# Kernel optimization log

Hardware: AMD Instinct MI355X
Metric: run time of the kernel (lower is better)

Reference implementation:

```python
import jax, jax.numpy as jnp
import numpy as np

B, T, D = 16, 2048, 256
WINDOW = 128


def setup_inputs() -> dict:
    key = jax.random.key(0)
    ks = jax.random.split(key, 6)
    scale = 1.0 / np.sqrt(D)
    return {
        "x": jax.random.normal(ks[0], (B, T, D), dtype=jnp.float32),
        "Wq": jax.random.normal(ks[1], (D, D), dtype=jnp.float32) * scale,
        "Wk": jax.random.normal(ks[2], (D, D), dtype=jnp.float32) * scale,
        "Wv": jax.random.normal(ks[3], (D, D), dtype=jnp.float32) * scale,
        "Wo": jax.random.normal(ks[4], (D, D), dtype=jnp.float32) * scale,
        "w_bias": jax.random.normal(ks[5], (T, T), dtype=jnp.float32) * 0.1,
        "window": WINDOW,
    }


def reference(x, Wq, Wk, Wv, Wo, w_bias, window):
    # x: [B,T,D]; w_bias: [T,T] learned pairwise position bias.
    T_ = x.shape[1]
    q = jnp.einsum("btd,de->bte", x, Wq)
    k = jnp.einsum("btd,de->bte", x, Wk)
    v = jnp.einsum("btd,de->bte", x, Wv)

    # AFT-Local: bias is zeroed outside the local band |t - t'| < window,
    # but ALL positions still contribute (with bias 0) to the weighted sum.
    idx = jnp.arange(T_)
    band = jnp.abs(idx[:, None] - idx[None, :]) < window  # [T,T] bool
    w_local = jnp.where(band, w_bias, 0.0)

    # Stable exponentials: the num/den ratio is invariant to per-row shifts
    # of w and per-(b,d) shifts of k.
    w_stable = w_local - jnp.max(w_local, axis=1, keepdims=True)
    k_stable = k - jnp.max(k, axis=1, keepdims=True)
    expw = jnp.exp(w_stable)  # [T,T]
    expk = jnp.exp(k_stable)  # [B,T,D]

    num = jnp.einsum("ts,bsd->btd", expw, expk * v)
    den = jnp.einsum("ts,bsd->btd", expw, expk)
    y = jax.nn.sigmoid(q) * (num / den)
    return jnp.einsum("btd,de->bte", y, Wo)
```

## Files before the change

### kernel.cpp

```cpp
#include <hip/hip_runtime.h>
#include <math.h>

#define B_ 16
#define T_ 2048
#define D_ 256
#define W_ 128
#define M_ (B_*T_)

typedef __attribute__((ext_vector_type(8))) short bf16x8;
typedef __attribute__((ext_vector_type(4))) float f32x4;
typedef unsigned short u16;

static __device__ __forceinline__ u16 f32_bf16_rne(float f) {
    unsigned int u = __float_as_uint(f);
    u += 0x7FFF + ((u >> 16) & 1);
    return (u16)(u >> 16);
}
static __device__ __forceinline__ float bf16_f32(u16 h) {
    return __uint_as_float(((unsigned int)h) << 16);
}

__global__ __launch_bounds__(256) void aft_split_wT(
    const float* __restrict__ Wq, const float* __restrict__ Wk,
    const float* __restrict__ Wv, const float* __restrict__ Wo,
    u16* __restrict__ Wth, u16* __restrict__ Wkl)
{
    const float* Ws[4] = {Wq, Wk, Wv, Wo};
    const float* W = Ws[blockIdx.x];
    const int n  = blockIdx.y * 16 + (threadIdx.x >> 4);
    const int k0 = (threadIdx.x & 15) * 16;
    size_t obase = ((size_t)blockIdx.x * 256 + n) * 256 + k0;
    #pragma unroll 4
    for (int j = 0; j < 16; ++j) {
        float v = W[(size_t)(k0 + j) * 256 + n];
        u16 h = f32_bf16_rne(v);
        Wth[obase + j] = h;
        if (blockIdx.x == 1)
            Wkl[(size_t)n * 256 + k0 + j] = f32_bf16_rne(v - bf16_f32(h));
    }
}

__global__ void aft_ewb(const float* __restrict__ wb, u16* __restrict__ EWb)
{
    const int t = blockIdx.x;
    const int j = threadIdx.x;
    const int s = (t & ~63) - 128 + j;
    const int dlt = s - t;
    float v = 0.f;
    if (s >= 0 && s < T_ && dlt > -W_ && dlt < W_)
        v = expf(wb[(size_t)t * T_ + s]) - 1.0f;
    EWb[(size_t)t * 320 + j] = f32_bf16_rne(v);
}

__global__ __launch_bounds__(256) void aft_qkv_mfma(
    const float* __restrict__ x,
    const u16* __restrict__ Wth, const u16* __restrict__ Wkl,
    u16* __restrict__ ekT, u16* __restrict__ sigqT)
{
    __shared__ alignas(16) u16 sm[20480];
    u16* Ah = sm;
    u16* Al = sm + 5120;
    u16* Bs = sm + 10240;
    u16* Tr = sm;

    const int tid  = threadIdx.x;
    const int row0 = blockIdx.x * 128;
    const int col0 = blockIdx.y * 64;
    const int b    = row0 >> 11;
    const int t0g  = row0 & (T_ - 1);
    const int lane = tid & 63;
    const int wid  = tid >> 6;
    const int wm   = (wid & 1) * 64;
    const int wn   = (wid >> 1) * 32;
    const int qd   = lane >> 4;
    const int r    = lane & 15;

    f32x4 accq[4][2], acck[4][2], accv[4][2];
    #pragma unroll
    for (int i = 0; i < 4; ++i)
        #pragma unroll
        for (int j = 0; j < 2; ++j) {
            accq[i][j] = (f32x4){0.f, 0.f, 0.f, 0.f};
            acck[i][j] = accq[i][j];
            accv[i][j] = accq[i][j];
        }

    const int am   = tid >> 1;
    const int akh  = (tid & 1) * 16;
    const int brow = tid >> 2;
    const int bseg = (tid & 3) * 8;

    for (int k0 = 0; k0 < D_; k0 += 32) {
        {
            size_t g = (size_t)(row0 + am) * D_ + k0 + akh;
            union { ushort4 s4[4]; u16 h[16]; } H, L;
            #pragma unroll
            for (int c = 0; c < 4; ++c) {
                float4 v = *(const float4*)&x[g + c * 4];
                float vv[4] = {v.x, v.y, v.z, v.w};
                #pragma unroll
                for (int e = 0; e < 4; ++e) {
                    u16 h = f32_bf16_rne(vv[e]);
                    H.h[c * 4 + e] = h;
                    L.h[c * 4 + e] = f32_bf16_rne(vv[e] - bf16_f32(h));
                }
            }
            *(ushort4*)&Ah[am * 40 + akh]      = H.s4[0];
            *(ushort4*)&Ah[am * 40 + akh + 4]  = H.s4[1];
            *(ushort4*)&Ah[am * 40 + akh + 8]  = H.s4[2];
            *(ushort4*)&Ah[am * 40 + akh + 12] = H.s4[3];
            *(ushort4*)&Al[am * 40 + akh]      = L.s4[0];
            *(ushort4*)&Al[am * 40 + akh + 4]  = L.s4[1];
            *(ushort4*)&Al[am * 40 + akh + 8]  = L.s4[2];
            *(ushort4*)&Al[am * 40 + akh + 12] = L.s4[3];
        }
        {
            size_t nrow = (size_t)(col0 + brow) * 256 + k0 + bseg;
            uint4 vq  = *(const uint4*)&Wth[nrow];
            uint4 vkh = *(const uint4*)&Wth[65536 + nrow];
            uint4 vkl = *(const uint4*)&Wkl[nrow];
            uint4 vv  = *(const uint4*)&Wth[2 * 65536 + nrow];
            *(uint4*)&Bs[0 * 2560 + brow * 40 + bseg] = vq;
            *(uint4*)&Bs[1 * 2560 + brow * 40 + bseg] = vkh;
            *(uint4*)&Bs[2 * 2560 + brow * 40 + bseg] = vkl;
            *(uint4*)&Bs[3 * 2560 + brow * 40 + bseg] = vv;
        }
        __syncthreads();

        bf16x8 ah[4], al[4];
        #pragma unroll
        for (int mf = 0; mf < 4; ++mf) {
            ah[mf] = *(const bf16x8*)&Ah[(wm + mf * 16 + r) * 40 + qd * 8];
            al[mf] = *(const bf16x8*)&Al[(wm + mf * 16 + r) * 40 + qd * 8];
        }
        #pragma unroll
        for (int nf = 0; nf < 2; ++nf) {
            int br = (wn + nf * 16 + r) * 40 + qd * 8;
            bf16x8 bq  = *(const bf16x8*)&Bs[br];
            bf16x8 bkh = *(const bf16x8*)&Bs[2560 + br];
            bf16x8 bkl = *(const bf16x8*)&Bs[5120 + br];
            bf16x8 bv  = *(const bf16x8*)&Bs[7680 + br];
            #pragma unroll
            for (int mf = 0; mf < 4; ++mf) {
                accq[mf][nf] = __builtin_amdgcn_mfma_f32_16x16x32_bf16(ah[mf], bq,  accq[mf][nf], 0, 0, 0);
                acck[mf][nf] = __builtin_amdgcn_mfma_f32_16x16x32_bf16(ah[mf], bkh, acck[mf][nf], 0, 0, 0);
                acck[mf][nf] = __builtin_amdgcn_mfma_f32_16x16x32_bf16(ah[mf], bkl, acck[mf][nf], 0, 0, 0);
                acck[mf][nf] = __builtin_amdgcn_mfma_f32_16x16x32_bf16(al[mf], bkh, acck[mf][nf], 0, 0, 0);
                accv[mf][nf] = __builtin_amdgcn_mfma_f32_16x16x32_bf16(ah[mf], bv,  accv[mf][nf], 0, 0, 0);
            }
        }
        __syncthreads();
    }

    const int dl_r = tid >> 2;
    const int tseg = (tid & 3) * 32;
    #pragma unroll
    for (int round = 0; round < 3; ++round) {
        __syncthreads();
        #pragma unroll
        for (int mf = 0; mf < 4; ++mf) {
            #pragma unroll
            for (int nf = 0; nf < 2; ++nf) {
                ushort4 o;
                float vals[4];
                #pragma unroll
                for (int reg = 0; reg < 4; ++reg) {
                    if (round == 0)      vals[reg] = expf(acck[mf][nf][reg]);
                    else if (round == 1) vals[reg] = expf(acck[mf][nf][reg]) * accv[mf][nf][reg];
                    else                 vals[reg] = 1.f / (1.f + expf(-accq[mf][nf][reg]));
                }
                o.x = f32_bf16_rne(vals[0]); o.y = f32_bf16_rne(vals[1]);
                o.z = f32_bf16_rne(vals[2]); o.w = f32_bf16_rne(vals[3]);
                int dl = wn + nf * 16 + r;
                int tt = wm + mf * 16 + qd * 4;
                *(ushort4*)&Tr[dl * 136 + tt] = o;
            }
        }
        __syncthreads();
        u16* dst;
        if (round == 0)      dst = ekT   + ((size_t)(b * 512 + col0 + dl_r)) * 2048;
        else if (round == 1) dst = ekT   + ((size_t)(b * 512 + 256 + col0 + dl_r)) * 2048;
        else                 dst = sigqT + ((size_t)(b * 256 + col0 + dl_r)) * 2048;
        dst += t0g + tseg;
        const u16* srcp = &Tr[dl_r * 136 + tseg];
        #pragma unroll
        for (int i = 0; i < 4; ++i)
            *(uint4*)&dst[i * 8] = *(const uint4*)&srcp[i * 8];
    }
}

__global__ __launch_bounds__(256) void aft_sums(
    const u16* __restrict__ ekT, float* __restrict__ Sk, float* __restrict__ Sv)
{
    const int wid  = threadIdx.x >> 6;
    const int lane = threadIdx.x & 63;
    const int row  = blockIdx.x * 4 + wid;
    const int b = row >> 9, n = row & 511;
    const u16* p = ekT + (size_t)row * 2048 + lane * 32;
    float s = 0.f;
    #pragma unroll
    for (int c = 0; c < 4; ++c) {
        union { uint4 v; u16 h[8]; } u;
        u.v = *(const uint4*)&p[c * 8];
        #pragma unroll
        for (int i = 0; i < 8; ++i) s += bf16_f32(u.h[i]);
    }
    #pragma unroll
    for (int off = 32; off >= 1; off >>= 1) s += __shfl_down(s, off, 64);
    if (lane == 0) {
        if (n < 256) Sk[b * 256 + n] = s;
        else         Sv[b * 256 + n - 256] = s;
    }
}

__global__ __launch_bounds__(256) void aft_band_mfma(
    const u16* __restrict__ EWb, const u16* __restrict__ ekT,
    const u16* __restrict__ sigqT,
    const float* __restrict__ Sk, const float* __restrict__ Sv,
    u16* __restrict__ yTD)
{
    __shared__ alignas(16) u16 sm[12800];
    u16* Aw  = sm;
    u16* Bkv = sm + 2560;

    const int tid  = threadIdx.x;
    const int t0   = blockIdx.x * 64;
    const int b    = blockIdx.y >> 1;
    const int dh   = (blockIdx.y & 1) * 128;
    const int lane = tid & 63;
    const int wid  = tid >> 6;
    const int wn   = wid * 32;
    const int qd   = lane >> 4;
    const int r    = lane & 15;

    f32x4 accn[4][2], accd[4][2];
    #pragma unroll
    for (int i = 0; i < 4; ++i)
        #pragma unroll
        for (int j = 0; j < 2; ++j) {
            accn[i][j] = (f32x4){0.f, 0.f, 0.f, 0.f};
            accd[i][j] = (f32x4){0.f, 0.f, 0.f, 0.f};
        }

    const int atl = tid >> 2;
    const int ak8 = (tid & 3) * 8;

    for (int c = 0; c < 10; ++c) {
        const int sc = t0 - 128 + c * 32;
        if (sc < 0 || sc >= T_) continue;
        __syncthreads();
        *(uint4*)&Aw[atl * 40 + ak8] =
            *(const uint4*)&EWb[(size_t)(t0 + atl) * 320 + c * 32 + ak8];
        #pragma unroll
        for (int rr = 0; rr < 4; ++rr) {
            int nl = rr * 64 + atl;
            int n  = (nl < 128) ? (dh + nl) : (256 + dh + nl - 128);
            *(uint4*)&Bkv[nl * 40 + ak8] =
                *(const uint4*)&ekT[((size_t)(b * 512) + n) * 2048 + sc + ak8];
        }
        __syncthreads();

        bf16x8 af[4];
        #pragma unroll
        for (int mf = 0; mf < 4; ++mf)
            af[mf] = *(const bf16x8*)&Aw[(mf * 16 + r) * 40 + qd * 8];
        #pragma unroll
        for (int nf = 0; nf < 2; ++nf) {
            bf16x8 be = *(const bf16x8*)&Bkv[(wn + nf * 16 + r) * 40 + qd * 8];
            bf16x8 bv = *(const bf16x8*)&Bkv[(128 + wn + nf * 16 + r) * 40 + qd * 8];
            #pragma unroll
            for (int mf = 0; mf < 4; ++mf) {
                accd[mf][nf] = __builtin_amdgcn_mfma_f32_16x16x32_bf16(af[mf], be, accd[mf][nf], 0, 0, 0);
                accn[mf][nf] = __builtin_amdgcn_mfma_f32_16x16x32_bf16(af[mf], bv, accn[mf][nf], 0, 0, 0);
            }
        }
    }

    __syncthreads();
    u16* Ly = sm;
    #pragma unroll
    for (int nf = 0; nf < 2; ++nf) {
        const int dl = wn + nf * 16 + r;
        const int d  = dh + dl;
        const float skq = Sk[(b << 8) + d];
        const float svq = Sv[(b << 8) + d];
        #pragma unroll
        for (int mf = 0; mf < 4; ++mf) {
            const int tt = t0 + mf * 16 + qd * 4;
            size_t off = ((size_t)(b << 8) + d) * 2048 + tt;
            ushort4 sg = *(const ushort4*)&sigqT[off];
            float s4[4] = {bf16_f32(sg.x), bf16_f32(sg.y), bf16_f32(sg.z), bf16_f32(sg.w)};
            #pragma unroll
            for (int reg = 0; reg < 4; ++reg) {
                float y = s4[reg] * (svq + accn[mf][nf][reg]) / (skq + accd[mf][nf][reg]);
                Ly[(mf * 16 + qd * 4 + reg) * 136 + dl] = f32_bf16_rne(y);
            }
        }
    }
    __syncthreads();
    {
        const int tl  = tid >> 2;
        const int ds4 = (tid & 3) * 32;
        u16* dst = yTD + ((size_t)b * 2048 + t0 + tl) * 256 + dh + ds4;
        #pragma unroll
        for (int i = 0; i < 4; ++i)
            *(uint4*)&dst[i * 8] = *(const uint4*)&Ly[tl * 136 + ds4 + i * 8];
    }
}

__global__ __launch_bounds__(256) void aft_out_mfma(
    const u16* __restrict__ yTD, const u16* __restrict__ Woth,
    float* __restrict__ out)
{
    __shared__ alignas(16) u16 sm[7680];
    u16* As = sm;
    u16* Bh = sm + 2560;

    const int tid  = threadIdx.x;
    const int row0 = blockIdx.x * 64;
    const int col0 = blockIdx.y * 128;
    const int lane = tid & 63;
    const int wid  = tid >> 6;
    const int wn   = wid * 32;
    const int qd   = lane >> 4;
    const int r    = lane & 15;

    f32x4 acc[4][2];
    #pragma unroll
    for (int i = 0; i < 4; ++i)
        #pragma unroll
        for (int j = 0; j < 2; ++j)
            acc[i][j] = (f32x4){0.f, 0.f, 0.f, 0.f};

    const int arow = tid >> 2;
    const int aseg = (tid & 3) * 8;
    const int brw  = tid >> 1;
    const int bsg  = (tid & 1) * 16;

    for (int k0 = 0; k0 < D_; k0 += 32) {
        {
            uint4 v = *(const uint4*)&yTD[(size_t)(row0 + arow) * 256 + k0 + aseg];
            *(uint4*)&As[arow * 40 + aseg] = v;
        }
        {
            size_t g = (size_t)(col0 + brw) * 256 + k0 + bsg;
            uint4 v0 = *(const uint4*)&Woth[g];
            uint4 v1 = *(const uint4*)&Woth[g + 8];
            *(uint4*)&Bh[brw * 40 + bsg]     = v0;
            *(uint4*)&Bh[brw * 40 + bsg + 8] = v1;
        }
        __syncthreads();

        bf16x8 af[4];
        #pragma unroll
        for (int mf = 0; mf < 4; ++mf)
            af[mf] = *(const bf16x8*)&As[(mf * 16 + r) * 40 + qd * 8];
        #pragma unroll
        for (int nf = 0; nf < 2; ++nf) {
            bf16x8 bh = *(const bf16x8*)&Bh[(wn + nf * 16 + r) * 40 + qd * 8];
            #pragma unroll
            for (int mf = 0; mf < 4; ++mf)
                acc[mf][nf] = __builtin_amdgcn_mfma_f32_16x16x32_bf16(af[mf], bh, acc[mf][nf], 0, 0, 0);
        }
        __syncthreads();
    }

    #pragma unroll
    for (int mf = 0; mf < 4; ++mf)
        #pragma unroll
        for (int nf = 0; nf < 2; ++nf)
            #pragma unroll
            for (int reg = 0; reg < 4; ++reg) {
                int mrow = row0 + mf * 16 + qd * 4 + reg;
                int ncol = col0 + wn + nf * 16 + r;
                out[(size_t)mrow * D_ + ncol] = acc[mf][nf][reg];
            }
}

extern "C" void kernel_launch(void* const* d_in, const int* in_sizes, int n_in,
                              void* d_out, int out_size, void* d_ws, size_t ws_size,
                              hipStream_t stream)
{
    const float* x  = (const float*)d_in[0];
    const float* Wq = (const float*)d_in[1];
    const float* Wk = (const float*)d_in[2];
    const float* Wv = (const float*)d_in[3];
    const float* Wo = (const float*)d_in[4];
    const float* wb = (const float*)d_in[5];

    u16* Wth   = (u16*)d_ws;
    u16* Wkl   = Wth + 262144;
    u16* EWb   = Wkl + 65536;
    u16* ekT   = EWb + 655360;
    u16* sigqT = ekT + 16777216;
    u16* yTD   = sigqT + 8388608;
    float* Sk  = (float*)(yTD + 8388608);
    float* Sv  = Sk + 4096;

    aft_split_wT<<<dim3(4, 16), 256, 0, stream>>>(Wq, Wk, Wv, Wo, Wth, Wkl);
    aft_ewb<<<dim3(T_), 320, 0, stream>>>(wb, EWb);
    aft_qkv_mfma<<<dim3(M_ / 128, 4), 256, 0, stream>>>(x, Wth, Wkl, ekT, sigqT);
    aft_sums<<<dim3(8192 / 4), 256, 0, stream>>>(ekT, Sk, Sv);
    aft_band_mfma<<<dim3(T_ / 64, B_ * 2), 256, 0, stream>>>(EWb, ekT, sigqT, Sk, Sv, yTD);
    aft_out_mfma<<<dim3(M_ / 64, 2), 256, 0, stream>>>(yTD, Wth + 3 * 65536, (float*)d_out);
}
```

Baseline: 201.9 us.

## Drop x low-part split in K projection and enlarge band-kernel tile to 128 rows

The QKV projection stops splitting x into high and low bf16 parts, which removes one MFMA per fragment and the Al shared-memory buffer. The exp and sigmoid epilogue is computed once into the accumulators instead of being recomputed inside each write-out round. The band kernel now processes 128 time rows per block with a 2x2 warp layout, loading the banded EWb rows with per-half chunk offsets and zero padding, so each ekT tile is reused by twice as many rows. Dropping the low part reduces the accuracy of k before exp, and the larger band tile does some extra work on zero-padded chunks while using more registers and LDS.

```diff
diff --git a/kernel.cpp b/kernel.cpp
--- a/kernel.cpp
+++ b/kernel.cpp
@@ -57,10 +57,9 @@
     const u16* __restrict__ Wth, const u16* __restrict__ Wkl,
     u16* __restrict__ ekT, u16* __restrict__ sigqT)
 {
-    __shared__ alignas(16) u16 sm[20480];
+    __shared__ alignas(16) u16 sm[15360];
     u16* Ah = sm;
-    u16* Al = sm + 5120;
-    u16* Bs = sm + 10240;
+    u16* Bs = sm + 5120;
     u16* Tr = sm;
 
     const int tid  = threadIdx.x;
@@ -93,26 +92,19 @@
     for (int k0 = 0; k0 < D_; k0 += 32) {
         {
             size_t g = (size_t)(row0 + am) * D_ + k0 + akh;
-            union { ushort4 s4[4]; u16 h[16]; } H, L;
+            union { ushort4 s4[4]; u16 h[16]; } H;
             #pragma unroll
             for (int c = 0; c < 4; ++c) {
                 float4 v = *(const float4*)&x[g + c * 4];
-                float vv[4] = {v.x, v.y, v.z, v.w};
-                #pragma unroll
-                for (int e = 0; e < 4; ++e) {
-                    u16 h = f32_bf16_rne(vv[e]);
-                    H.h[c * 4 + e] = h;
-                    L.h[c * 4 + e] = f32_bf16_rne(vv[e] - bf16_f32(h));
-                }
+                H.h[c * 4 + 0] = f32_bf16_rne(v.x);
+                H.h[c * 4 + 1] = f32_bf16_rne(v.y);
+                H.h[c * 4 + 2] = f32_bf16_rne(v.z);
+                H.h[c * 4 + 3] = f32_bf16_rne(v.w);
             }
             *(ushort4*)&Ah[am * 40 + akh]      = H.s4[0];
             *(ushort4*)&Ah[am * 40 + akh + 4]  = H.s4[1];
             *(ushort4*)&Ah[am * 40 + akh + 8]  = H.s4[2];
             *(ushort4*)&Ah[am * 40 + akh + 12] = H.s4[3];
-            *(ushort4*)&Al[am * 40 + akh]      = L.s4[0];
-            *(ushort4*)&Al[am * 40 + akh + 4]  = L.s4[1];
-            *(ushort4*)&Al[am * 40 + akh + 8]  = L.s4[2];
-            *(ushort4*)&Al[am * 40 + akh + 12] = L.s4[3];
         }
         {
             size_t nrow = (size_t)(col0 + brow) * 256 + k0 + bseg;
@@ -127,12 +119,10 @@
         }
         __syncthreads();
 
-        bf16x8 ah[4], al[4];
-        #pragma unroll
-        for (int mf = 0; mf < 4; ++mf) {
+        bf16x8 ah[4];
+        #pragma unroll
+        for (int mf = 0; mf < 4; ++mf)
             ah[mf] = *(const bf16x8*)&Ah[(wm + mf * 16 + r) * 40 + qd * 8];
-            al[mf] = *(const bf16x8*)&Al[(wm + mf * 16 + r) * 40 + qd * 8];
-        }
         #pragma unroll
         for (int nf = 0; nf < 2; ++nf) {
             int br = (wn + nf * 16 + r) * 40 + qd * 8;
@@ -145,12 +135,23 @@
                 accq[mf][nf] = __builtin_amdgcn_mfma_f32_16x16x32_bf16(ah[mf], bq,  accq[mf][nf], 0, 0, 0);
                 acck[mf][nf] = __builtin_amdgcn_mfma_f32_16x16x32_bf16(ah[mf], bkh, acck[mf][nf], 0, 0, 0);
                 acck[mf][nf] = __builtin_amdgcn_mfma_f32_16x16x32_bf16(ah[mf], bkl, acck[mf][nf], 0, 0, 0);
-                acck[mf][nf] = __builtin_amdgcn_mfma_f32_16x16x32_bf16(al[mf], bkh, acck[mf][nf], 0, 0, 0);
                 accv[mf][nf] = __builtin_amdgcn_mfma_f32_16x16x32_bf16(ah[mf], bv,  accv[mf][nf], 0, 0, 0);
             }
         }
         __syncthreads();
     }
+
+    #pragma unroll
+    for (int mf = 0; mf < 4; ++mf)
+        #pragma unroll
+        for (int nf = 0; nf < 2; ++nf)
+            #pragma unroll
+            for (int reg = 0; reg < 4; ++reg) {
+                float e = expf(acck[mf][nf][reg]);
+                acck[mf][nf][reg] = e;
+                accv[mf][nf][reg] = e * accv[mf][nf][reg];
+                accq[mf][nf][reg] = 1.f / (1.f + expf(-accq[mf][nf][reg]));
+            }
 
     const int dl_r = tid >> 2;
     const int tseg = (tid & 3) * 32;
@@ -161,16 +162,11 @@
         for (int mf = 0; mf < 4; ++mf) {
             #pragma unroll
             for (int nf = 0; nf < 2; ++nf) {
+                const f32x4* src = (round == 0) ? &acck[mf][nf]
+                                 : (round == 1) ? &accv[mf][nf] : &accq[mf][nf];
                 ushort4 o;
-                float vals[4];
-                #pragma unroll
-                for (int reg = 0; reg < 4; ++reg) {
-                    if (round == 0)      vals[reg] = expf(acck[mf][nf][reg]);
-                    else if (round == 1) vals[reg] = expf(acck[mf][nf][reg]) * accv[mf][nf][reg];
-                    else                 vals[reg] = 1.f / (1.f + expf(-accq[mf][nf][reg]));
-                }
-                o.x = f32_bf16_rne(vals[0]); o.y = f32_bf16_rne(vals[1]);
-                o.z = f32_bf16_rne(vals[2]); o.w = f32_bf16_rne(vals[3]);
+                o.x = f32_bf16_rne((*src)[0]); o.y = f32_bf16_rne((*src)[1]);
+                o.z = f32_bf16_rne((*src)[2]); o.w = f32_bf16_rne((*src)[3]);
                 int dl = wn + nf * 16 + r;
                 int tt = wm + mf * 16 + qd * 4;
                 *(ushort4*)&Tr[dl * 136 + tt] = o;
@@ -219,25 +215,26 @@
     const float* __restrict__ Sk, const float* __restrict__ Sv,
     u16* __restrict__ yTD)
 {
-    __shared__ alignas(16) u16 sm[12800];
+    __shared__ alignas(16) u16 sm[17408];
     u16* Aw  = sm;
-    u16* Bkv = sm + 2560;
+    u16* Bkv = sm + 5120;
 
     const int tid  = threadIdx.x;
-    const int t0   = blockIdx.x * 64;
+    const int t0   = blockIdx.x * 128;
     const int b    = blockIdx.y >> 1;
     const int dh   = (blockIdx.y & 1) * 128;
     const int lane = tid & 63;
     const int wid  = tid >> 6;
-    const int wn   = wid * 32;
+    const int wt   = (wid & 1) * 64;
+    const int wd   = (wid >> 1) * 64;
     const int qd   = lane >> 4;
     const int r    = lane & 15;
 
-    f32x4 accn[4][2], accd[4][2];
+    f32x4 accn[4][4], accd[4][4];
     #pragma unroll
     for (int i = 0; i < 4; ++i)
         #pragma unroll
-        for (int j = 0; j < 2; ++j) {
+        for (int j = 0; j < 4; ++j) {
             accn[i][j] = (f32x4){0.f, 0.f, 0.f, 0.f};
             accd[i][j] = (f32x4){0.f, 0.f, 0.f, 0.f};
         }
@@ -245,12 +242,21 @@
     const int atl = tid >> 2;
     const int ak8 = (tid & 3) * 8;
 
-    for (int c = 0; c < 10; ++c) {
+    for (int c = 0; c < 12; ++c) {
         const int sc = t0 - 128 + c * 32;
         if (sc < 0 || sc >= T_) continue;
         __syncthreads();
-        *(uint4*)&Aw[atl * 40 + ak8] =
-            *(const uint4*)&EWb[(size_t)(t0 + atl) * 320 + c * 32 + ak8];
+        #pragma unroll
+        for (int i = 0; i < 2; ++i) {
+            int e  = tid + i * 256;
+            int tl = e >> 2;
+            int sg = (e & 3) * 8;
+            int c2 = c - 2 * (tl >> 6);
+            uint4 v = {0u, 0u, 0u, 0u};
+            if (c2 >= 0 && c2 < 10)
+                v = *(const uint4*)&EWb[(size_t)(t0 + tl) * 320 + c2 * 32 + sg];
+            *(uint4*)&Aw[tl * 40 + sg] = v;
+        }
         #pragma unroll
         for (int rr = 0; rr < 4; ++rr) {
             int nl = rr * 64 + atl;
@@ -263,15 +269,15 @@
         bf16x8 af[4];
         #pragma unroll
         for (int mf = 0; mf < 4; ++mf)
-            af[mf] = *(const bf16x8*)&Aw[(mf * 16 + r) * 40 + qd * 8];
-        #pragma unroll
-        for (int nf = 0; nf < 2; ++nf) {
-            bf16x8 be = *(const bf16x8*)&Bkv[(wn + nf * 16 + r) * 40 + qd * 8];
-            bf16x8 bv = *(const bf16x8*)&Bkv[(128 + wn + nf * 16 + r) * 40 + qd * 8];
+            af[mf] = *(const bf16x8*)&Aw[(wt + mf * 16 + r) * 40 + qd * 8];
+        #pragma unroll
+        for (int df = 0; df < 4; ++df) {
+            bf16x8 be = *(const bf16x8*)&Bkv[(wd + df * 16 + r) * 40 + qd * 8];
+            bf16x8 bv = *(const bf16x8*)&Bkv[(128 + wd + df * 16 + r) * 40 + qd * 8];
             #pragma unroll
             for (int mf = 0; mf < 4; ++mf) {
-                accd[mf][nf] = __builtin_amdgcn_mfma_f32_16x16x32_bf16(af[mf], be, accd[mf][nf], 0, 0, 0);
-                accn[mf][nf] = __builtin_amdgcn_mfma_f32_16x16x32_bf16(af[mf], bv, accn[mf][nf], 0, 0, 0);
+                accd[mf][df] = __builtin_amdgcn_mfma_f32_16x16x32_bf16(af[mf], be, accd[mf][df], 0, 0, 0);
+                accn[mf][df] = __builtin_amdgcn_mfma_f32_16x16x32_bf16(af[mf], bv, accn[mf][df], 0, 0, 0);
             }
         }
     }
@@ -279,31 +285,31 @@
     __syncthreads();
     u16* Ly = sm;
     #pragma unroll
-    for (int nf = 0; nf < 2; ++nf) {
-        const int dl = wn + nf * 16 + r;
+    for (int df = 0; df < 4; ++df) {
+        const int dl = wd + df * 16 + r;
         const int d  = dh + dl;
         const float skq = Sk[(b << 8) + d];
         const float svq = Sv[(b << 8) + d];
         #pragma unroll
         for (int mf = 0; mf < 4; ++mf) {
-            const int tt = t0 + mf * 16 + qd * 4;
+            const int tt = t0 + wt + mf * 16 + qd * 4;
             size_t off = ((size_t)(b << 8) + d) * 2048 + tt;
             ushort4 sg = *(const ushort4*)&sigqT[off];
             float s4[4] = {bf16_f32(sg.x), bf16_f32(sg.y), bf16_f32(sg.z), bf16_f32(sg.w)};
             #pragma unroll
             for (int reg = 0; reg < 4; ++reg) {
-                float y = s4[reg] * (svq + accn[mf][nf][reg]) / (skq + accd[mf][nf][reg]);
-                Ly[(mf * 16 + qd * 4 + reg) * 136 + dl] = f32_bf16_rne(y);
+                float y = s4[reg] * (svq + accn[mf][df][reg]) / (skq + accd[mf][df][reg]);
+                Ly[(wt + mf * 16 + qd * 4 + reg) * 136 + dl] = f32_bf16_rne(y);
             }
         }
     }
     __syncthreads();
     {
-        const int tl  = tid >> 2;
-        const int ds4 = (tid & 3) * 32;
+        const int tl  = tid >> 1;
+        const int ds4 = (tid & 1) * 64;
         u16* dst = yTD + ((size_t)b * 2048 + t0 + tl) * 256 + dh + ds4;
         #pragma unroll
-        for (int i = 0; i < 4; ++i)
+        for (int i = 0; i < 8; ++i)
             *(uint4*)&dst[i * 8] = *(const uint4*)&Ly[tl * 136 + ds4 + i * 8];
     }
 }
@@ -401,6 +407,6 @@
     aft_ewb<<<dim3(T_), 320, 0, stream>>>(wb, EWb);
     aft_qkv_mfma<<<dim3(M_ / 128, 4), 256, 0, stream>>>(x, Wth, Wkl, ekT, sigqT);
     aft_sums<<<dim3(8192 / 4), 256, 0, stream>>>(ekT, Sk, Sv);
-    aft_band_mfma<<<dim3(T_ / 64, B_ * 2), 256, 0, stream>>>(EWb, ekT, sigqT, Sk, Sv, yTD);
+    aft_band_mfma<<<dim3(T_ / 128, B_ * 2), 256, 0, stream>>>(EWb, ekT, sigqT, Sk, Sv, yTD);
     aft_out_mfma<<<dim3(M_ / 64, 2), 256, 0, stream>>>(yTD, Wth + 3 * 65536, (float*)d_out);
 }
```

Result: slower. 208.7 us (+3.3%).
